# Performance work log

Hardware: AMD Instinct MI355X
Metric: run time of the kernel (lower is better)

Reference implementation:

```python
import jax, jax.numpy as jnp
import numpy as np

WINDOW_SIZE = 8
NUM_HEADS = 6
SHIFT_SIZE = 0


def rel_pos_log(ws):
    # torch.meshgrid default is 'ij' indexing
    coords = jnp.stack(jnp.meshgrid(jnp.arange(ws), jnp.arange(ws), indexing='ij'))  # [2,ws,ws]
    flat = coords.reshape(2, -1)                      # [2, N]
    rel = flat[:, :, None] - flat[:, None, :]          # [2, N, N]
    rel = rel.transpose(1, 2, 0).astype(jnp.float32)   # [N, N, 2]
    return jnp.sign(rel) * jnp.log1p(jnp.abs(rel))


def setup_inputs() -> dict:
    key = jax.random.key(0)
    k0, k1, k2, k3 = jax.random.split(key, 4)
    B_, N, dim, H = 2048, WINDOW_SIZE * WINDOW_SIZE, 192, NUM_HEADS
    qkv = jax.random.normal(k0, (B_, N, 3 * dim), dtype=jnp.float32)
    qkv_mfif = jax.random.normal(k1, (B_, N, 3 * dim), dtype=jnp.float32)
    W1 = jax.random.normal(k2, (2, 256), dtype=jnp.float32) * 0.1
    b1 = jnp.zeros((256,), dtype=jnp.float32)
    W2 = jax.random.normal(k3, (256, H), dtype=jnp.float32) * 0.1
    b2 = jnp.zeros((H,), dtype=jnp.float32)
    return {"qkv": qkv, "qkv_mfif": qkv_mfif, "W1": W1, "b1": b1,
            "W2": W2, "b2": b2, "trainingTag": 2}


def _split_heads(t, H):
    B_, N, C3 = t.shape
    dim = C3 // 3
    hd = dim // H
    t = t.reshape(B_, N, 3, H, hd).transpose(2, 0, 3, 1, 4)  # [3, B_, H, N, hd]
    return t[0], t[1], t[2]


def _forward(qkv, qkv_mfif, W1, b1, W2, b2, trainingTag):
    sg = jax.lax.stop_gradient
    H = NUM_HEADS
    B_, N, C3 = qkv.shape
    dim = C3 // 3
    hd = dim // H
    scale = hd ** (-0.5)

    q, k, v = _split_heads(qkv, H)
    qm, km, vm = _split_heads(qkv_mfif, H)

    # relative position bias from tiny MLP: [N,N,2] -> [N,N,H] -> [H,N,N]
    rp = rel_pos_log(WINDOW_SIZE)
    bias = jax.nn.relu(rp @ W1 + b1) @ W2 + b2
    bias = bias.transpose(2, 0, 1)[None]  # [1,H,N,N]

    if trainingTag == 2:
        q = sg(q * scale)
        qm = qm * scale
        if SHIFT_SIZE == 0:
            attn = sg(jnp.einsum('bhnd,bhmd->bhnm', qm, k))
        else:
            attn = sg(jnp.einsum('bhnd,bhmd->bhnm', q, k))
        attn_m = jnp.einsum('bhnd,bhmd->bhnm', qm, km)
        attn = sg(jax.nn.softmax(attn + sg(bias), axis=-1))
        attn_m = jax.nn.softmax(attn_m + bias, axis=-1)
        x_ivif = sg(jnp.einsum('bhnm,bhmd->bhnd', attn, v).transpose(0, 2, 1, 3).reshape(B_, N, dim))
        x_mfif = jnp.einsum('bhnm,bhmd->bhnd', attn_m, vm).transpose(0, 2, 1, 3).reshape(B_, N, dim)
    else:  # trainingTag == 1
        q = q * scale
        qm = sg(qm * scale)
        attn = jnp.einsum('bhnd,bhmd->bhnm', q, k)
        if SHIFT_SIZE == 0:
            attn_m = sg(jnp.einsum('bhnd,bhmd->bhnm', q, km))
        else:
            attn_m = sg(jnp.einsum('bhnd,bhmd->bhnm', qm, km))
        attn = jax.nn.softmax(attn + bias, axis=-1)
        attn_m = sg(jax.nn.softmax(attn_m + bias, axis=-1))
        x_ivif = jnp.einsum('bhnm,bhmd->bhnd', attn, v).transpose(0, 2, 1, 3).reshape(B_, N, dim)
        x_mfif = sg(jnp.einsum('bhnm,bhmd->bhnd', attn_m, vm).transpose(0, 2, 1, 3).reshape(B_, N, dim))
    return x_ivif, x_mfif


def reference(qkv, qkv_mfif, W1, b1, W2, b2, trainingTag):
    return _forward(qkv, qkv_mfif, W1, b1, W2, b2, trainingTag)
```

## Files before the change

### kernel.cpp

```cpp
#include <hip/hip_runtime.h>


typedef float  f32x4  __attribute__((ext_vector_type(4)));
typedef short  bf16x8 __attribute__((ext_vector_type(8)));
typedef unsigned short u16x8 __attribute__((ext_vector_type(8)));
typedef unsigned short u16x4 __attribute__((ext_vector_type(4)));

__device__ __forceinline__ unsigned short f2bf(float f) {
  unsigned int u = __builtin_bit_cast(unsigned int, f);
  unsigned int r = (u + 0x7FFFu + ((u >> 16) & 1u)) >> 16;
  return (unsigned short)r;
}

__global__ void bias_mlp_kernel(const float* __restrict__ W1,
                                const float* __restrict__ b1,
                                const float* __restrict__ W2,
                                const float* __restrict__ b2,
                                float* __restrict__ bias_ws) {
  int idx  = blockIdx.x * 256 + threadIdx.x;
  int reg  = idx & 3;
  int lane = (idx >> 2) & 63;
  int tile = (idx >> 8) & 15;
  int h    = idx >> 12;
  int mt = tile >> 2, nt = tile & 3;
  int n = nt * 16 + (lane & 15);
  int m = mt * 16 + (lane >> 4) * 4 + reg;
  float dr = (float)((n >> 3) - (m >> 3));
  float dc = (float)((n & 7) - (m & 7));
  float fr = copysignf(log1pf(fabsf(dr)), dr);
  float fc = copysignf(log1pf(fabsf(dc)), dc);
  float acc = b2[h];
  for (int jj = 0; jj < 256; ++jj) {
    float hid = fmaf(fr, W1[jj], fmaf(fc, W1[256 + jj], b1[jj]));
    hid = fmaxf(hid, 0.0f);
    acc = fmaf(hid, W2[jj * 6 + h], acc);
  }
  bias_ws[idx] = acc;
}

__global__ __launch_bounds__(256, 6)
void wattn_kernel(const float* __restrict__ qkv,
                  const float* __restrict__ mfif,
                  const float* __restrict__ bias_ws,
                  const int*   __restrict__ tagp,
                  float* __restrict__ out) {
  const int bid  = blockIdx.x;
  const int h    = bid % 6;
  const int b    = bid / 6;
  const int tid  = threadIdx.x;
  const int lane = tid & 63;
  const int w    = tid >> 6;
  const int j    = lane & 15;
  const int g    = lane >> 4;

  __shared__ unsigned short k_s [64][36];
  __shared__ unsigned short km_s[64][36];
  __shared__ unsigned short vT_s[2][32][66];
  __shared__ unsigned short P_s [64][66];

  const int tag = *tagp;
  const float* qsrc = (tag == 2) ? mfif : qkv;
  const size_t base = (size_t)b * 36864;
  const float scale = 0.17677669529663687f;

  bf16x8 bq;
  {
    const float* pq = qsrc + base + (size_t)(16 * w + j) * 576 + h * 32 + g * 8;
    f32x4 q0 = *(const f32x4*)pq;
    f32x4 q1 = *(const f32x4*)(pq + 4);
    u16x8 oq;
#pragma unroll
    for (int e = 0; e < 4; ++e) {
      oq[e]     = f2bf(q0[e] * scale);
      oq[e + 4] = f2bf(q1[e] * scale);
    }
    bq = __builtin_bit_cast(bf16x8, oq);
  }

  {
    const int n = tid >> 2, seg = tid & 3;
    const float* pk = qkv  + base + (size_t)n * 576 + 192 + h * 32 + seg * 8;
    const float* pm = mfif + base + (size_t)n * 576 + 192 + h * 32 + seg * 8;
    f32x4 k0 = *(const f32x4*)pk;  f32x4 k1 = *(const f32x4*)(pk + 4);
    f32x4 m0 = *(const f32x4*)pm;  f32x4 m1 = *(const f32x4*)(pm + 4);
    u16x8 ok, om;
#pragma unroll
    for (int e = 0; e < 4; ++e) {
      ok[e] = f2bf(k0[e]);  ok[e + 4] = f2bf(k1[e]);
      om[e] = f2bf(m0[e]);  om[e + 4] = f2bf(m1[e]);
    }
    *(u16x8*)&k_s [n][seg * 8] = ok;
    *(u16x8*)&km_s[n][seg * 8] = om;
  }
  {
    const int d  = tid & 31;
    const int m0 = (tid >> 5) * 8;
    const float* pv  = qkv  + base + 384 + h * 32 + d;
    const float* pvm = mfif + base + 384 + h * 32 + d;
    u16x8 ov, om;
#pragma unroll
    for (int e = 0; e < 8; ++e) {
      ov[e] = f2bf(pv [(size_t)(m0 + e) * 576]);
      om[e] = f2bf(pvm[(size_t)(m0 + e) * 576]);
    }
    *(u16x8*)&vT_s[0][d][m0] = ov;
    *(u16x8*)&vT_s[1][d][m0] = om;
  }

  f32x4 bias4[4];
#pragma unroll
  for (int mt = 0; mt < 4; ++mt)
    bias4[mt] = *(const f32x4*)&bias_ws[(((h * 16) + mt * 4 + w) * 64 + lane) * 4];

  __syncthreads();

#pragma unroll
  for (int s = 0; s < 2; ++s) {
    const unsigned short (*Ks)[36] = (s == 0) ? k_s : km_s;

    f32x4 acc[4];
#pragma unroll
    for (int mt = 0; mt < 4; ++mt) {
      bf16x8 ak = *(const bf16x8*)&Ks[mt * 16 + j][g * 8];
      acc[mt] = __builtin_amdgcn_mfma_f32_16x16x32_bf16(ak, bq, bias4[mt], 0, 0, 0);
    }

    float mx = -3.0e38f;
#pragma unroll
    for (int mt = 0; mt < 4; ++mt)
#pragma unroll
      for (int r = 0; r < 4; ++r) mx = fmaxf(mx, acc[mt][r]);
    mx = fmaxf(mx, __shfl_xor(mx, 16));
    mx = fmaxf(mx, __shfl_xor(mx, 32));
    float p[16];
    float sum = 0.0f;
#pragma unroll
    for (int mt = 0; mt < 4; ++mt)
#pragma unroll
      for (int r = 0; r < 4; ++r) {
        float e = __expf(acc[mt][r] - mx);
        p[mt * 4 + r] = e;
        sum += e;
      }
    sum += __shfl_xor(sum, 16);
    sum += __shfl_xor(sum, 32);
    const float inv = 1.0f / sum;

#pragma unroll
    for (int mt = 0; mt < 4; ++mt) {
      u16x4 pw;
#pragma unroll
      for (int r = 0; r < 4; ++r) pw[r] = f2bf(p[mt * 4 + r] * inv);
      *(u16x4*)&P_s[16 * w + j][mt * 16 + g * 4] = pw;
    }

    f32x4 xo[2] = {{0.f, 0.f, 0.f, 0.f}, {0.f, 0.f, 0.f, 0.f}};
#pragma unroll
    for (int kt = 0; kt < 2; ++kt) {
      bf16x8 ap = *(const bf16x8*)&P_s[16 * w + j][kt * 32 + g * 8];
#pragma unroll
      for (int dt = 0; dt < 2; ++dt) {
        bf16x8 bv = *(const bf16x8*)&vT_s[s][16 * dt + j][kt * 32 + g * 8];
        xo[dt] = __builtin_amdgcn_mfma_f32_16x16x32_bf16(ap, bv, xo[dt], 0, 0, 0);
      }
    }

    float* ob = out + (size_t)s * 25165824 + (size_t)b * 12288 + h * 32;
#pragma unroll
    for (int dt = 0; dt < 2; ++dt)
#pragma unroll
      for (int r = 0; r < 4; ++r)
        ob[(16 * w + g * 4 + r) * 192 + dt * 16 + j] = xo[dt][r];
  }
}

extern "C" void kernel_launch(void* const* d_in, const int* in_sizes, int n_in,
                              void* d_out, int out_size, void* d_ws, size_t ws_size,
                              hipStream_t stream) {
  const float* qkv  = (const float*)d_in[0];
  const float* mfif = (const float*)d_in[1];
  const float* W1   = (const float*)d_in[2];
  const float* b1   = (const float*)d_in[3];
  const float* W2   = (const float*)d_in[4];
  const float* b2   = (const float*)d_in[5];
  const int*   tag  = (const int*)d_in[6];
  float* out     = (float*)d_out;
  float* bias_ws = (float*)d_ws;

  hipLaunchKernelGGL(bias_mlp_kernel, dim3(96), dim3(256), 0, stream,
                     W1, b1, W2, b2, bias_ws);
  hipLaunchKernelGGL(wattn_kernel, dim3(12288), dim3(256), 0, stream,
                     qkv, mfif, bias_ws, tag, out);
}
```

Baseline: 157.4 us.

## Process all heads per block with register-prefetched next-head loads

Each block now handles one window and loops over all six heads, cutting the grid from 12288 to 2048 blocks. Global loads for the next head are issued into registers before the current head's compute, software-pipelining memory latency behind the MFMA and softmax work. Launch bounds drop to 4 blocks per SM to allow more registers for the prefetch buffers. The cost is lower occupancy, less parallelism across heads, and two extra barriers per head.

```diff
diff --git a/kernel.cpp b/kernel.cpp
--- a/kernel.cpp
+++ b/kernel.cpp
@@ -38,15 +38,12 @@
   bias_ws[idx] = acc;
 }
 
-__global__ __launch_bounds__(256, 6)
+__global__ __launch_bounds__(256, 4)
 void wattn_kernel(const float* __restrict__ qkv,
                   const float* __restrict__ mfif,
                   const float* __restrict__ bias_ws,
                   const int*   __restrict__ tagp,
                   float* __restrict__ out) {
-  const int bid  = blockIdx.x;
-  const int h    = bid % 6;
-  const int b    = bid / 6;
   const int tid  = threadIdx.x;
   const int lane = tid & 63;
   const int w    = tid >> 6;
@@ -60,117 +57,136 @@
 
   const int tag = *tagp;
   const float* qsrc = (tag == 2) ? mfif : qkv;
-  const size_t base = (size_t)b * 36864;
+  const size_t base = (size_t)blockIdx.x * 36864;
   const float scale = 0.17677669529663687f;
 
-  bf16x8 bq;
-  {
-    const float* pq = qsrc + base + (size_t)(16 * w + j) * 576 + h * 32 + g * 8;
-    f32x4 q0 = *(const f32x4*)pq;
-    f32x4 q1 = *(const f32x4*)(pq + 4);
-    u16x8 oq;
+  const int q_row = 16 * w + j;
+  const int n_k   = tid >> 2, seg = tid & 3;
+  const int d_v   = tid & 31, m0_v = (tid >> 5) * 8;
+
+  const float* qrow_p  = qsrc + base + (size_t)q_row * 576 + g * 8;
+  const float* krow_p  = qkv  + base + (size_t)n_k * 576 + 192 + seg * 8;
+  const float* mrow_p  = mfif + base + (size_t)n_k * 576 + 192 + seg * 8;
+  const float* vcol_p  = qkv  + base + 384 + d_v;
+  const float* vmcol_p = mfif + base + 384 + d_v;
+
+  f32x4 qA, qB, kA, kB, mA, mB;
+  float vv[8], vmv[8];
+
+  auto ISSUE = [&](int hh) {
+    const float* pq = qrow_p + hh * 32;
+    qA = *(const f32x4*)pq;        qB = *(const f32x4*)(pq + 4);
+    const float* pk = krow_p + hh * 32;
+    kA = *(const f32x4*)pk;        kB = *(const f32x4*)(pk + 4);
+    const float* pm = mrow_p + hh * 32;
+    mA = *(const f32x4*)pm;        mB = *(const f32x4*)(pm + 4);
+    const float* pv  = vcol_p  + hh * 32;
+    const float* pvm = vmcol_p + hh * 32;
+#pragma unroll
+    for (int e = 0; e < 8; ++e) {
+      vv[e]  = pv [(size_t)(m0_v + e) * 576];
+      vmv[e] = pvm[(size_t)(m0_v + e) * 576];
+    }
+  };
+
+  ISSUE(0);
+
+#pragma unroll 1
+  for (int hh = 0; hh < 6; ++hh) {
+    bf16x8 bq;
+    {
+      u16x8 oq;
+#pragma unroll
+      for (int e = 0; e < 4; ++e) {
+        oq[e]     = f2bf(qA[e] * scale);
+        oq[e + 4] = f2bf(qB[e] * scale);
+      }
+      bq = __builtin_bit_cast(bf16x8, oq);
+    }
+    u16x8 ok, om, ov, ovm;
 #pragma unroll
     for (int e = 0; e < 4; ++e) {
-      oq[e]     = f2bf(q0[e] * scale);
-      oq[e + 4] = f2bf(q1[e] * scale);
-    }
-    bq = __builtin_bit_cast(bf16x8, oq);
-  }
-
-  {
-    const int n = tid >> 2, seg = tid & 3;
-    const float* pk = qkv  + base + (size_t)n * 576 + 192 + h * 32 + seg * 8;
-    const float* pm = mfif + base + (size_t)n * 576 + 192 + h * 32 + seg * 8;
-    f32x4 k0 = *(const f32x4*)pk;  f32x4 k1 = *(const f32x4*)(pk + 4);
-    f32x4 m0 = *(const f32x4*)pm;  f32x4 m1 = *(const f32x4*)(pm + 4);
-    u16x8 ok, om;
-#pragma unroll
-    for (int e = 0; e < 4; ++e) {
-      ok[e] = f2bf(k0[e]);  ok[e + 4] = f2bf(k1[e]);
-      om[e] = f2bf(m0[e]);  om[e + 4] = f2bf(m1[e]);
-    }
-    *(u16x8*)&k_s [n][seg * 8] = ok;
-    *(u16x8*)&km_s[n][seg * 8] = om;
-  }
-  {
-    const int d  = tid & 31;
-    const int m0 = (tid >> 5) * 8;
-    const float* pv  = qkv  + base + 384 + h * 32 + d;
-    const float* pvm = mfif + base + 384 + h * 32 + d;
-    u16x8 ov, om;
+      ok[e] = f2bf(kA[e]);  ok[e + 4] = f2bf(kB[e]);
+      om[e] = f2bf(mA[e]);  om[e + 4] = f2bf(mB[e]);
+    }
 #pragma unroll
     for (int e = 0; e < 8; ++e) {
-      ov[e] = f2bf(pv [(size_t)(m0 + e) * 576]);
-      om[e] = f2bf(pvm[(size_t)(m0 + e) * 576]);
-    }
-    *(u16x8*)&vT_s[0][d][m0] = ov;
-    *(u16x8*)&vT_s[1][d][m0] = om;
-  }
-
-  f32x4 bias4[4];
-#pragma unroll
-  for (int mt = 0; mt < 4; ++mt)
-    bias4[mt] = *(const f32x4*)&bias_ws[(((h * 16) + mt * 4 + w) * 64 + lane) * 4];
-
-  __syncthreads();
-
-#pragma unroll
-  for (int s = 0; s < 2; ++s) {
-    const unsigned short (*Ks)[36] = (s == 0) ? k_s : km_s;
-
-    f32x4 acc[4];
-#pragma unroll
-    for (int mt = 0; mt < 4; ++mt) {
-      bf16x8 ak = *(const bf16x8*)&Ks[mt * 16 + j][g * 8];
-      acc[mt] = __builtin_amdgcn_mfma_f32_16x16x32_bf16(ak, bq, bias4[mt], 0, 0, 0);
-    }
-
-    float mx = -3.0e38f;
+      ov[e]  = f2bf(vv[e]);
+      ovm[e] = f2bf(vmv[e]);
+    }
+
+    __syncthreads();
+    *(u16x8*)&k_s [n_k][seg * 8] = ok;
+    *(u16x8*)&km_s[n_k][seg * 8] = om;
+    *(u16x8*)&vT_s[0][d_v][m0_v] = ov;
+    *(u16x8*)&vT_s[1][d_v][m0_v] = ovm;
+    __syncthreads();
+
+    if (hh < 5) ISSUE(hh + 1);
+
+    f32x4 bias4[4];
 #pragma unroll
     for (int mt = 0; mt < 4; ++mt)
-#pragma unroll
-      for (int r = 0; r < 4; ++r) mx = fmaxf(mx, acc[mt][r]);
-    mx = fmaxf(mx, __shfl_xor(mx, 16));
-    mx = fmaxf(mx, __shfl_xor(mx, 32));
-    float p[16];
-    float sum = 0.0f;
-#pragma unroll
-    for (int mt = 0; mt < 4; ++mt)
-#pragma unroll
-      for (int r = 0; r < 4; ++r) {
-        float e = __expf(acc[mt][r] - mx);
-        p[mt * 4 + r] = e;
-        sum += e;
-      }
-    sum += __shfl_xor(sum, 16);
-    sum += __shfl_xor(sum, 32);
-    const float inv = 1.0f / sum;
-
-#pragma unroll
-    for (int mt = 0; mt < 4; ++mt) {
-      u16x4 pw;
-#pragma unroll
-      for (int r = 0; r < 4; ++r) pw[r] = f2bf(p[mt * 4 + r] * inv);
-      *(u16x4*)&P_s[16 * w + j][mt * 16 + g * 4] = pw;
-    }
-
-    f32x4 xo[2] = {{0.f, 0.f, 0.f, 0.f}, {0.f, 0.f, 0.f, 0.f}};
-#pragma unroll
-    for (int kt = 0; kt < 2; ++kt) {
-      bf16x8 ap = *(const bf16x8*)&P_s[16 * w + j][kt * 32 + g * 8];
-#pragma unroll
-      for (int dt = 0; dt < 2; ++dt) {
-        bf16x8 bv = *(const bf16x8*)&vT_s[s][16 * dt + j][kt * 32 + g * 8];
-        xo[dt] = __builtin_amdgcn_mfma_f32_16x16x32_bf16(ap, bv, xo[dt], 0, 0, 0);
-      }
-    }
-
-    float* ob = out + (size_t)s * 25165824 + (size_t)b * 12288 + h * 32;
-#pragma unroll
-    for (int dt = 0; dt < 2; ++dt)
-#pragma unroll
-      for (int r = 0; r < 4; ++r)
-        ob[(16 * w + g * 4 + r) * 192 + dt * 16 + j] = xo[dt][r];
+      bias4[mt] = *(const f32x4*)&bias_ws[(((hh * 16) + mt * 4 + w) * 64 + lane) * 4];
+
+#pragma unroll
+    for (int s = 0; s < 2; ++s) {
+      const unsigned short (*Ks)[36] = (s == 0) ? k_s : km_s;
+
+      f32x4 acc[4];
+#pragma unroll
+      for (int mt = 0; mt < 4; ++mt) {
+        bf16x8 ak = *(const bf16x8*)&Ks[mt * 16 + j][g * 8];
+        acc[mt] = __builtin_amdgcn_mfma_f32_16x16x32_bf16(ak, bq, bias4[mt], 0, 0, 0);
+      }
+
+      float mx = -3.0e38f;
+#pragma unroll
+      for (int mt = 0; mt < 4; ++mt)
+#pragma unroll
+        for (int r = 0; r < 4; ++r) mx = fmaxf(mx, acc[mt][r]);
+      mx = fmaxf(mx, __shfl_xor(mx, 16));
+      mx = fmaxf(mx, __shfl_xor(mx, 32));
+      float p[16];
+      float sum = 0.0f;
+#pragma unroll
+      for (int mt = 0; mt < 4; ++mt)
+#pragma unroll
+        for (int r = 0; r < 4; ++r) {
+          float e = __expf(acc[mt][r] - mx);
+          p[mt * 4 + r] = e;
+          sum += e;
+        }
+      sum += __shfl_xor(sum, 16);
+      sum += __shfl_xor(sum, 32);
+      const float inv = 1.0f / sum;
+
+#pragma unroll
+      for (int mt = 0; mt < 4; ++mt) {
+        u16x4 pw;
+#pragma unroll
+        for (int r = 0; r < 4; ++r) pw[r] = f2bf(p[mt * 4 + r] * inv);
+        *(u16x4*)&P_s[16 * w + j][mt * 16 + g * 4] = pw;
+      }
+
+      f32x4 xo[2] = {{0.f, 0.f, 0.f, 0.f}, {0.f, 0.f, 0.f, 0.f}};
+#pragma unroll
+      for (int kt = 0; kt < 2; ++kt) {
+        bf16x8 ap = *(const bf16x8*)&P_s[16 * w + j][kt * 32 + g * 8];
+#pragma unroll
+        for (int dt = 0; dt < 2; ++dt) {
+          bf16x8 bv = *(const bf16x8*)&vT_s[s][16 * dt + j][kt * 32 + g * 8];
+          xo[dt] = __builtin_amdgcn_mfma_f32_16x16x32_bf16(ap, bv, xo[dt], 0, 0, 0);
+        }
+      }
+
+      float* ob = out + (size_t)s * 25165824 + (size_t)blockIdx.x * 12288 + hh * 32;
+#pragma unroll
+      for (int dt = 0; dt < 2; ++dt)
+#pragma unroll
+        for (int r = 0; r < 4; ++r)
+          ob[(16 * w + g * 4 + r) * 192 + dt * 16 + j] = xo[dt][r];
+    }
   }
 }
 
@@ -189,6 +205,6 @@
 
   hipLaunchKernelGGL(bias_mlp_kernel, dim3(96), dim3(256), 0, stream,
                      W1, b1, W2, b2, bias_ws);
-  hipLaunchKernelGGL(wattn_kernel, dim3(12288), dim3(256), 0, stream,
+  hipLaunchKernelGGL(wattn_kernel, dim3(2048), dim3(256), 0, stream,
                      qkv, mfif, bias_ws, tag, out);
 }
```

Result: slower. 176.9 us (+12.4%).

## Load K straight into MFMA registers and defer softmax normalization

Applied to the files above, without the earlier changes.

The K and K_mfif tiles are no longer staged through shared memory: each lane loads its own K fragment from global memory, converts it to bf16 and feeds it directly into the QK^T MFMA. V loads are issued before the softmax so their latency overlaps it. The row max is dropped, unnormalized exponentials are written to P, and the reciprocal of the row sum is applied to the output after the PV MFMA. Together with the smaller shared-memory footprint and a launch bound raised from 6 to 8 waves, this aims for more overlap and higher occupancy, at the cost of overflow risk in exp when logits are large.

```diff
diff --git a/kernel.cpp b/kernel.cpp
--- a/kernel.cpp
+++ b/kernel.cpp
@@ -38,7 +38,7 @@
   bias_ws[idx] = acc;
 }
 
-__global__ __launch_bounds__(256, 6)
+__global__ __launch_bounds__(256, 8)
 void wattn_kernel(const float* __restrict__ qkv,
                   const float* __restrict__ mfif,
                   const float* __restrict__ bias_ws,
@@ -53,124 +53,165 @@
   const int j    = lane & 15;
   const int g    = lane >> 4;
 
-  __shared__ unsigned short k_s [64][36];
-  __shared__ unsigned short km_s[64][36];
   __shared__ unsigned short vT_s[2][32][66];
   __shared__ unsigned short P_s [64][66];
+  __shared__ __align__(16) float sums_s[2][64];
 
   const int tag = *tagp;
   const float* qsrc = (tag == 2) ? mfif : qkv;
   const size_t base = (size_t)b * 36864;
   const float scale = 0.17677669529663687f;
 
-  bf16x8 bq;
+  f32x4 qA, qB;
   {
     const float* pq = qsrc + base + (size_t)(16 * w + j) * 576 + h * 32 + g * 8;
-    f32x4 q0 = *(const f32x4*)pq;
-    f32x4 q1 = *(const f32x4*)(pq + 4);
-    u16x8 oq;
-#pragma unroll
-    for (int e = 0; e < 4; ++e) {
-      oq[e]     = f2bf(q0[e] * scale);
-      oq[e + 4] = f2bf(q1[e] * scale);
-    }
-    bq = __builtin_bit_cast(bf16x8, oq);
-  }
-
-  {
-    const int n = tid >> 2, seg = tid & 3;
-    const float* pk = qkv  + base + (size_t)n * 576 + 192 + h * 32 + seg * 8;
-    const float* pm = mfif + base + (size_t)n * 576 + 192 + h * 32 + seg * 8;
-    f32x4 k0 = *(const f32x4*)pk;  f32x4 k1 = *(const f32x4*)(pk + 4);
-    f32x4 m0 = *(const f32x4*)pm;  f32x4 m1 = *(const f32x4*)(pm + 4);
-    u16x8 ok, om;
-#pragma unroll
-    for (int e = 0; e < 4; ++e) {
-      ok[e] = f2bf(k0[e]);  ok[e + 4] = f2bf(k1[e]);
-      om[e] = f2bf(m0[e]);  om[e + 4] = f2bf(m1[e]);
-    }
-    *(u16x8*)&k_s [n][seg * 8] = ok;
-    *(u16x8*)&km_s[n][seg * 8] = om;
-  }
-  {
-    const int d  = tid & 31;
-    const int m0 = (tid >> 5) * 8;
-    const float* pv  = qkv  + base + 384 + h * 32 + d;
-    const float* pvm = mfif + base + 384 + h * 32 + d;
-    u16x8 ov, om;
-#pragma unroll
-    for (int e = 0; e < 8; ++e) {
-      ov[e] = f2bf(pv [(size_t)(m0 + e) * 576]);
-      om[e] = f2bf(pvm[(size_t)(m0 + e) * 576]);
-    }
-    *(u16x8*)&vT_s[0][d][m0] = ov;
-    *(u16x8*)&vT_s[1][d][m0] = om;
-  }
-
+    qA = *(const f32x4*)pq;
+    qB = *(const f32x4*)(pq + 4);
+  }
   f32x4 bias4[4];
 #pragma unroll
   for (int mt = 0; mt < 4; ++mt)
     bias4[mt] = *(const f32x4*)&bias_ws[(((h * 16) + mt * 4 + w) * 64 + lane) * 4];
 
-  __syncthreads();
-
-#pragma unroll
-  for (int s = 0; s < 2; ++s) {
-    const unsigned short (*Ks)[36] = (s == 0) ? k_s : km_s;
-
-    f32x4 acc[4];
+  const float* kb0 = qkv + base + 192 + h * 32 + (size_t)j * 576 + g * 8;
+
+  bf16x8 bq;
+  {
+    u16x8 oq;
+#pragma unroll
+    for (int e = 0; e < 4; ++e) {
+      oq[e]     = f2bf(qA[e] * scale);
+      oq[e + 4] = f2bf(qB[e] * scale);
+    }
+    bq = __builtin_bit_cast(bf16x8, oq);
+  }
+
+  f32x4 acc[4];
+#pragma unroll
+  for (int mt = 0; mt < 4; ++mt) {
+    f32x4 a0 = *(const f32x4*)(kb0 + (size_t)mt * 9216);
+    f32x4 a1 = *(const f32x4*)(kb0 + (size_t)mt * 9216 + 4);
+    u16x8 ok;
+#pragma unroll
+    for (int e = 0; e < 4; ++e) { ok[e] = f2bf(a0[e]); ok[e + 4] = f2bf(a1[e]); }
+    acc[mt] = __builtin_amdgcn_mfma_f32_16x16x32_bf16(
+        __builtin_bit_cast(bf16x8, ok), bq, bias4[mt], 0, 0, 0);
+  }
+
+  const int d_v = tid & 31, m0_v = (tid >> 5) * 8;
+  const float* pv  = qkv  + base + 384 + h * 32 + d_v;
+  const float* pvm = mfif + base + 384 + h * 32 + d_v;
+  float vv[8], vmv[8];
+#pragma unroll
+  for (int e = 0; e < 8; ++e) vv[e]  = pv [(size_t)(m0_v + e) * 576];
+#pragma unroll
+  for (int e = 0; e < 8; ++e) vmv[e] = pvm[(size_t)(m0_v + e) * 576];
+
+  {
+    float t0 = 0.f, t1 = 0.f, t2 = 0.f, t3 = 0.f;
 #pragma unroll
     for (int mt = 0; mt < 4; ++mt) {
-      bf16x8 ak = *(const bf16x8*)&Ks[mt * 16 + j][g * 8];
-      acc[mt] = __builtin_amdgcn_mfma_f32_16x16x32_bf16(ak, bq, bias4[mt], 0, 0, 0);
-    }
-
-    float mx = -3.0e38f;
-#pragma unroll
-    for (int mt = 0; mt < 4; ++mt)
-#pragma unroll
-      for (int r = 0; r < 4; ++r) mx = fmaxf(mx, acc[mt][r]);
-    mx = fmaxf(mx, __shfl_xor(mx, 16));
-    mx = fmaxf(mx, __shfl_xor(mx, 32));
-    float p[16];
-    float sum = 0.0f;
-#pragma unroll
-    for (int mt = 0; mt < 4; ++mt)
-#pragma unroll
-      for (int r = 0; r < 4; ++r) {
-        float e = __expf(acc[mt][r] - mx);
-        p[mt * 4 + r] = e;
-        sum += e;
-      }
+      float e0 = __expf(acc[mt][0]);
+      float e1 = __expf(acc[mt][1]);
+      float e2 = __expf(acc[mt][2]);
+      float e3 = __expf(acc[mt][3]);
+      u16x4 pw;
+      pw[0] = f2bf(e0); pw[1] = f2bf(e1); pw[2] = f2bf(e2); pw[3] = f2bf(e3);
+      *(u16x4*)&P_s[16 * w + j][mt * 16 + g * 4] = pw;
+      t0 += e0; t1 += e1; t2 += e2; t3 += e3;
+    }
+    float sum = (t0 + t1) + (t2 + t3);
     sum += __shfl_xor(sum, 16);
     sum += __shfl_xor(sum, 32);
-    const float inv = 1.0f / sum;
-
-#pragma unroll
-    for (int mt = 0; mt < 4; ++mt) {
-      u16x4 pw;
-#pragma unroll
-      for (int r = 0; r < 4; ++r) pw[r] = f2bf(p[mt * 4 + r] * inv);
-      *(u16x4*)&P_s[16 * w + j][mt * 16 + g * 4] = pw;
-    }
-
+    if (g == 0) sums_s[0][16 * w + j] = sum;
+  }
+
+  {
+    u16x8 ov, om;
+#pragma unroll
+    for (int e = 0; e < 8; ++e) { ov[e] = f2bf(vv[e]); om[e] = f2bf(vmv[e]); }
+    *(u16x8*)&vT_s[0][d_v][m0_v] = ov;
+    *(u16x8*)&vT_s[1][d_v][m0_v] = om;
+  }
+  __syncthreads();
+
+  {
     f32x4 xo[2] = {{0.f, 0.f, 0.f, 0.f}, {0.f, 0.f, 0.f, 0.f}};
 #pragma unroll
     for (int kt = 0; kt < 2; ++kt) {
       bf16x8 ap = *(const bf16x8*)&P_s[16 * w + j][kt * 32 + g * 8];
 #pragma unroll
       for (int dt = 0; dt < 2; ++dt) {
-        bf16x8 bv = *(const bf16x8*)&vT_s[s][16 * dt + j][kt * 32 + g * 8];
+        bf16x8 bv = *(const bf16x8*)&vT_s[0][16 * dt + j][kt * 32 + g * 8];
         xo[dt] = __builtin_amdgcn_mfma_f32_16x16x32_bf16(ap, bv, xo[dt], 0, 0, 0);
       }
     }
-
-    float* ob = out + (size_t)s * 25165824 + (size_t)b * 12288 + h * 32;
+    f32x4 sm = *(const f32x4*)&sums_s[0][16 * w + 4 * g];
+    float inv[4];
+#pragma unroll
+    for (int r = 0; r < 4; ++r) inv[r] = __builtin_amdgcn_rcpf(sm[r]);
+    float* ob = out + (size_t)b * 12288 + h * 32;
 #pragma unroll
     for (int dt = 0; dt < 2; ++dt)
 #pragma unroll
       for (int r = 0; r < 4; ++r)
-        ob[(16 * w + g * 4 + r) * 192 + dt * 16 + j] = xo[dt][r];
+        ob[(16 * w + g * 4 + r) * 192 + dt * 16 + j] = xo[dt][r] * inv[r];
+  }
+
+  {
+    const float* kb1 = mfif + base + 192 + h * 32 + (size_t)j * 576 + g * 8;
+    f32x4 acm[4];
+#pragma unroll
+    for (int mt = 0; mt < 4; ++mt) {
+      f32x4 a0 = *(const f32x4*)(kb1 + (size_t)mt * 9216);
+      f32x4 a1 = *(const f32x4*)(kb1 + (size_t)mt * 9216 + 4);
+      u16x8 ok;
+#pragma unroll
+      for (int e = 0; e < 4; ++e) { ok[e] = f2bf(a0[e]); ok[e + 4] = f2bf(a1[e]); }
+      acm[mt] = __builtin_amdgcn_mfma_f32_16x16x32_bf16(
+          __builtin_bit_cast(bf16x8, ok), bq, bias4[mt], 0, 0, 0);
+    }
+    float t0 = 0.f, t1 = 0.f, t2 = 0.f, t3 = 0.f;
+    u16x4 pw1[4];
+#pragma unroll
+    for (int mt = 0; mt < 4; ++mt) {
+      float e0 = __expf(acm[mt][0]);
+      float e1 = __expf(acm[mt][1]);
+      float e2 = __expf(acm[mt][2]);
+      float e3 = __expf(acm[mt][3]);
+      pw1[mt][0] = f2bf(e0); pw1[mt][1] = f2bf(e1);
+      pw1[mt][2] = f2bf(e2); pw1[mt][3] = f2bf(e3);
+      t0 += e0; t1 += e1; t2 += e2; t3 += e3;
+    }
+    float sum = (t0 + t1) + (t2 + t3);
+    sum += __shfl_xor(sum, 16);
+    sum += __shfl_xor(sum, 32);
+    if (g == 0) sums_s[1][16 * w + j] = sum;
+
+#pragma unroll
+    for (int mt = 0; mt < 4; ++mt)
+      *(u16x4*)&P_s[16 * w + j][mt * 16 + g * 4] = pw1[mt];
+
+    f32x4 xo[2] = {{0.f, 0.f, 0.f, 0.f}, {0.f, 0.f, 0.f, 0.f}};
+#pragma unroll
+    for (int kt = 0; kt < 2; ++kt) {
+      bf16x8 ap = *(const bf16x8*)&P_s[16 * w + j][kt * 32 + g * 8];
+#pragma unroll
+      for (int dt = 0; dt < 2; ++dt) {
+        bf16x8 bv = *(const bf16x8*)&vT_s[1][16 * dt + j][kt * 32 + g * 8];
+        xo[dt] = __builtin_amdgcn_mfma_f32_16x16x32_bf16(ap, bv, xo[dt], 0, 0, 0);
+      }
+    }
+    f32x4 sm = *(const f32x4*)&sums_s[1][16 * w + 4 * g];
+    float inv[4];
+#pragma unroll
+    for (int r = 0; r < 4; ++r) inv[r] = __builtin_amdgcn_rcpf(sm[r]);
+    float* ob = out + 25165824 + (size_t)b * 12288 + h * 32;
+#pragma unroll
+    for (int dt = 0; dt < 2; ++dt)
+#pragma unroll
+      for (int r = 0; r < 4; ++r)
+        ob[(16 * w + g * 4 + r) * 192 + dt * 16 + j] = xo[dt][r] * inv[r];
   }
 }
 
```

Measured after the change: 266.7 us. +69.5%, slower.

## Process two heads per block with wider loads and deferred softmax normalization

Applied to the files above, without the earlier changes.

Each block now handles a pair of heads. This halves the grid and lets K and V rows be loaded as contiguous 64-float spans with float4 loads. The block index is remapped so neighbouring work lands on the same XCD. Softmax no longer subtracts the row max; normalization by the reciprocal of the row sum is moved to the output store, with row sums passed through shared memory. The aim is to cut memory-transaction and ALU overhead in a bandwidth-bound kernel, at the cost of lower occupancy and a risk of exp overflow for large scores.

```diff
diff --git a/kernel.cpp b/kernel.cpp
--- a/kernel.cpp
+++ b/kernel.cpp
@@ -38,139 +38,163 @@
   bias_ws[idx] = acc;
 }
 
-__global__ __launch_bounds__(256, 6)
+__global__ __launch_bounds__(256, 3)
 void wattn_kernel(const float* __restrict__ qkv,
                   const float* __restrict__ mfif,
                   const float* __restrict__ bias_ws,
                   const int*   __restrict__ tagp,
                   float* __restrict__ out) {
-  const int bid  = blockIdx.x;
-  const int h    = bid % 6;
-  const int b    = bid / 6;
+  const int nb   = blockIdx.x;
+  const int orig = (nb & 7) * 768 + (nb >> 3);
+  const int b    = orig / 3;
+  const int hp   = orig - 3 * b;
   const int tid  = threadIdx.x;
   const int lane = tid & 63;
   const int w    = tid >> 6;
   const int j    = lane & 15;
   const int g    = lane >> 4;
 
-  __shared__ unsigned short k_s [64][36];
-  __shared__ unsigned short km_s[64][36];
-  __shared__ unsigned short vT_s[2][32][66];
+  __shared__ unsigned short k_s [2][64][36];
+  __shared__ unsigned short km_s[2][64][36];
+  __shared__ unsigned short vT_s[2][2][32][72];
   __shared__ unsigned short P_s [64][66];
+  __shared__ __align__(16) float sums_s[2][64];
 
   const int tag = *tagp;
   const float* qsrc = (tag == 2) ? mfif : qkv;
   const size_t base = (size_t)b * 36864;
   const float scale = 0.17677669529663687f;
 
-  bf16x8 bq;
+  const int rl  = lane >> 4;
+  const int c16 = lane & 15;
+  const float* kbp = qkv  + base + (size_t)(16 * w + rl) * 576 + 192 + 64 * hp + c16 * 4;
+  const float* mbp = mfif + base + (size_t)(16 * w + rl) * 576 + 192 + 64 * hp + c16 * 4;
+  f32x4 kf0 = *(const f32x4*)(kbp);
+  f32x4 kf1 = *(const f32x4*)(kbp + 4 * 576);
+  f32x4 kf2 = *(const f32x4*)(kbp + 8 * 576);
+  f32x4 kf3 = *(const f32x4*)(kbp + 12 * 576);
+  f32x4 mf0 = *(const f32x4*)(mbp);
+  f32x4 mf1 = *(const f32x4*)(mbp + 4 * 576);
+  f32x4 mf2 = *(const f32x4*)(mbp + 8 * 576);
+  f32x4 mf3 = *(const f32x4*)(mbp + 12 * 576);
+
+  const float* vbp  = qkv  + base + (size_t)(16 * w) * 576 + 384 + 64 * hp + lane;
+  const float* vmbp = mfif + base + (size_t)(16 * w) * 576 + 384 + 64 * hp + lane;
+  float vv[16], vmv[16];
+#pragma unroll
+  for (int e = 0; e < 16; ++e) {
+    vv[e]  = vbp [(size_t)e * 576];
+    vmv[e] = vmbp[(size_t)e * 576];
+  }
+
+  const int hl = c16 >> 3;
+  const int cc = (c16 & 7) * 4;
   {
-    const float* pq = qsrc + base + (size_t)(16 * w + j) * 576 + h * 32 + g * 8;
-    f32x4 q0 = *(const f32x4*)pq;
-    f32x4 q1 = *(const f32x4*)(pq + 4);
-    u16x8 oq;
-#pragma unroll
-    for (int e = 0; e < 4; ++e) {
-      oq[e]     = f2bf(q0[e] * scale);
-      oq[e + 4] = f2bf(q1[e] * scale);
+    u16x4 t0, t1;
+#pragma unroll
+    for (int e = 0; e < 4; ++e) { t0[e] = f2bf(kf0[e]); t1[e] = f2bf(mf0[e]); }
+    *(u16x4*)&k_s [hl][16 * w + 0 + rl][cc] = t0;
+    *(u16x4*)&km_s[hl][16 * w + 0 + rl][cc] = t1;
+#pragma unroll
+    for (int e = 0; e < 4; ++e) { t0[e] = f2bf(kf1[e]); t1[e] = f2bf(mf1[e]); }
+    *(u16x4*)&k_s [hl][16 * w + 4 + rl][cc] = t0;
+    *(u16x4*)&km_s[hl][16 * w + 4 + rl][cc] = t1;
+#pragma unroll
+    for (int e = 0; e < 4; ++e) { t0[e] = f2bf(kf2[e]); t1[e] = f2bf(mf2[e]); }
+    *(u16x4*)&k_s [hl][16 * w + 8 + rl][cc] = t0;
+    *(u16x4*)&km_s[hl][16 * w + 8 + rl][cc] = t1;
+#pragma unroll
+    for (int e = 0; e < 4; ++e) { t0[e] = f2bf(kf3[e]); t1[e] = f2bf(mf3[e]); }
+    *(u16x4*)&k_s [hl][16 * w + 12 + rl][cc] = t0;
+    *(u16x4*)&km_s[hl][16 * w + 12 + rl][cc] = t1;
+  }
+  {
+    const int hv = lane >> 5, dd = lane & 31;
+    u16x8 a0, a1, b0, b1;
+#pragma unroll
+    for (int e = 0; e < 8; ++e) {
+      a0[e] = f2bf(vv[e]);      a1[e] = f2bf(vv[8 + e]);
+      b0[e] = f2bf(vmv[e]);     b1[e] = f2bf(vmv[8 + e]);
     }
-    bq = __builtin_bit_cast(bf16x8, oq);
-  }
-
-  {
-    const int n = tid >> 2, seg = tid & 3;
-    const float* pk = qkv  + base + (size_t)n * 576 + 192 + h * 32 + seg * 8;
-    const float* pm = mfif + base + (size_t)n * 576 + 192 + h * 32 + seg * 8;
-    f32x4 k0 = *(const f32x4*)pk;  f32x4 k1 = *(const f32x4*)(pk + 4);
-    f32x4 m0 = *(const f32x4*)pm;  f32x4 m1 = *(const f32x4*)(pm + 4);
-    u16x8 ok, om;
-#pragma unroll
-    for (int e = 0; e < 4; ++e) {
-      ok[e] = f2bf(k0[e]);  ok[e + 4] = f2bf(k1[e]);
-      om[e] = f2bf(m0[e]);  om[e + 4] = f2bf(m1[e]);
+    *(u16x8*)&vT_s[hv][0][dd][16 * w]     = a0;
+    *(u16x8*)&vT_s[hv][0][dd][16 * w + 8] = a1;
+    *(u16x8*)&vT_s[hv][1][dd][16 * w]     = b0;
+    *(u16x8*)&vT_s[hv][1][dd][16 * w + 8] = b1;
+  }
+  __syncthreads();
+
+#pragma unroll
+  for (int h2 = 0; h2 < 2; ++h2) {
+    const int h = 2 * hp + h2;
+
+    bf16x8 bq;
+    {
+      const float* pq = qsrc + base + (size_t)(16 * w + j) * 576 + h * 32 + g * 8;
+      f32x4 qA = *(const f32x4*)pq;
+      f32x4 qB = *(const f32x4*)(pq + 4);
+      u16x8 oq;
+#pragma unroll
+      for (int e = 0; e < 4; ++e) {
+        oq[e]     = f2bf(qA[e] * scale);
+        oq[e + 4] = f2bf(qB[e] * scale);
+      }
+      bq = __builtin_bit_cast(bf16x8, oq);
     }
-    *(u16x8*)&k_s [n][seg * 8] = ok;
-    *(u16x8*)&km_s[n][seg * 8] = om;
-  }
-  {
-    const int d  = tid & 31;
-    const int m0 = (tid >> 5) * 8;
-    const float* pv  = qkv  + base + 384 + h * 32 + d;
-    const float* pvm = mfif + base + 384 + h * 32 + d;
-    u16x8 ov, om;
-#pragma unroll
-    for (int e = 0; e < 8; ++e) {
-      ov[e] = f2bf(pv [(size_t)(m0 + e) * 576]);
-      om[e] = f2bf(pvm[(size_t)(m0 + e) * 576]);
+    f32x4 bias4[4];
+#pragma unroll
+    for (int mt = 0; mt < 4; ++mt)
+      bias4[mt] = *(const f32x4*)&bias_ws[(((h * 16) + mt * 4 + w) * 64 + lane) * 4];
+
+#pragma unroll
+    for (int s = 0; s < 2; ++s) {
+      const unsigned short (*Ks)[36] = (s == 0) ? k_s[h2] : km_s[h2];
+
+      f32x4 acc[4];
+#pragma unroll
+      for (int mt = 0; mt < 4; ++mt) {
+        bf16x8 ak = *(const bf16x8*)&Ks[mt * 16 + j][g * 8];
+        acc[mt] = __builtin_amdgcn_mfma_f32_16x16x32_bf16(ak, bq, bias4[mt], 0, 0, 0);
+      }
+
+      float t0 = 0.f, t1 = 0.f, t2 = 0.f, t3 = 0.f;
+#pragma unroll
+      for (int mt = 0; mt < 4; ++mt) {
+        float e0 = __expf(acc[mt][0]);
+        float e1 = __expf(acc[mt][1]);
+        float e2 = __expf(acc[mt][2]);
+        float e3 = __expf(acc[mt][3]);
+        u16x4 pw;
+        pw[0] = f2bf(e0); pw[1] = f2bf(e1); pw[2] = f2bf(e2); pw[3] = f2bf(e3);
+        *(u16x4*)&P_s[16 * w + j][mt * 16 + g * 4] = pw;
+        t0 += e0; t1 += e1; t2 += e2; t3 += e3;
+      }
+      float sum = (t0 + t1) + (t2 + t3);
+      sum += __shfl_xor(sum, 16);
+      sum += __shfl_xor(sum, 32);
+      if (g == 0) sums_s[s][16 * w + j] = sum;
+
+      f32x4 xo[2] = {{0.f, 0.f, 0.f, 0.f}, {0.f, 0.f, 0.f, 0.f}};
+#pragma unroll
+      for (int kt = 0; kt < 2; ++kt) {
+        bf16x8 ap = *(const bf16x8*)&P_s[16 * w + j][kt * 32 + g * 8];
+#pragma unroll
+        for (int dt = 0; dt < 2; ++dt) {
+          bf16x8 bv = *(const bf16x8*)&vT_s[h2][s][16 * dt + j][kt * 32 + g * 8];
+          xo[dt] = __builtin_amdgcn_mfma_f32_16x16x32_bf16(ap, bv, xo[dt], 0, 0, 0);
+        }
+      }
+
+      f32x4 sm = *(const f32x4*)&sums_s[s][16 * w + 4 * g];
+      float inv[4];
+#pragma unroll
+      for (int r = 0; r < 4; ++r) inv[r] = __builtin_amdgcn_rcpf(sm[r]);
+      float* ob = out + (size_t)s * 25165824 + (size_t)b * 12288 + h * 32;
+#pragma unroll
+      for (int dt = 0; dt < 2; ++dt)
+#pragma unroll
+        for (int r = 0; r < 4; ++r)
+          ob[(16 * w + g * 4 + r) * 192 + dt * 16 + j] = xo[dt][r] * inv[r];
     }
-    *(u16x8*)&vT_s[0][d][m0] = ov;
-    *(u16x8*)&vT_s[1][d][m0] = om;
-  }
-
-  f32x4 bias4[4];
-#pragma unroll
-  for (int mt = 0; mt < 4; ++mt)
-    bias4[mt] = *(const f32x4*)&bias_ws[(((h * 16) + mt * 4 + w) * 64 + lane) * 4];
-
-  __syncthreads();
-
-#pragma unroll
-  for (int s = 0; s < 2; ++s) {
-    const unsigned short (*Ks)[36] = (s == 0) ? k_s : km_s;
-
-    f32x4 acc[4];
-#pragma unroll
-    for (int mt = 0; mt < 4; ++mt) {
-      bf16x8 ak = *(const bf16x8*)&Ks[mt * 16 + j][g * 8];
-      acc[mt] = __builtin_amdgcn_mfma_f32_16x16x32_bf16(ak, bq, bias4[mt], 0, 0, 0);
-    }
-
-    float mx = -3.0e38f;
-#pragma unroll
-    for (int mt = 0; mt < 4; ++mt)
-#pragma unroll
-      for (int r = 0; r < 4; ++r) mx = fmaxf(mx, acc[mt][r]);
-    mx = fmaxf(mx, __shfl_xor(mx, 16));
-    mx = fmaxf(mx, __shfl_xor(mx, 32));
-    float p[16];
-    float sum = 0.0f;
-#pragma unroll
-    for (int mt = 0; mt < 4; ++mt)
-#pragma unroll
-      for (int r = 0; r < 4; ++r) {
-        float e = __expf(acc[mt][r] - mx);
-        p[mt * 4 + r] = e;
-        sum += e;
-      }
-    sum += __shfl_xor(sum, 16);
-    sum += __shfl_xor(sum, 32);
-    const float inv = 1.0f / sum;
-
-#pragma unroll
-    for (int mt = 0; mt < 4; ++mt) {
-      u16x4 pw;
-#pragma unroll
-      for (int r = 0; r < 4; ++r) pw[r] = f2bf(p[mt * 4 + r] * inv);
-      *(u16x4*)&P_s[16 * w + j][mt * 16 + g * 4] = pw;
-    }
-
-    f32x4 xo[2] = {{0.f, 0.f, 0.f, 0.f}, {0.f, 0.f, 0.f, 0.f}};
-#pragma unroll
-    for (int kt = 0; kt < 2; ++kt) {
-      bf16x8 ap = *(const bf16x8*)&P_s[16 * w + j][kt * 32 + g * 8];
-#pragma unroll
-      for (int dt = 0; dt < 2; ++dt) {
-        bf16x8 bv = *(const bf16x8*)&vT_s[s][16 * dt + j][kt * 32 + g * 8];
-        xo[dt] = __builtin_amdgcn_mfma_f32_16x16x32_bf16(ap, bv, xo[dt], 0, 0, 0);
-      }
-    }
-
-    float* ob = out + (size_t)s * 25165824 + (size_t)b * 12288 + h * 32;
-#pragma unroll
-    for (int dt = 0; dt < 2; ++dt)
-#pragma unroll
-      for (int r = 0; r < 4; ++r)
-        ob[(16 * w + g * 4 + r) * 192 + dt * 16 + j] = xo[dt][r];
   }
 }
 
@@ -189,6 +213,6 @@
 
   hipLaunchKernelGGL(bias_mlp_kernel, dim3(96), dim3(256), 0, stream,
                      W1, b1, W2, b2, bias_ws);
-  hipLaunchKernelGGL(wattn_kernel, dim3(12288), dim3(256), 0, stream,
+  hipLaunchKernelGGL(wattn_kernel, dim3(6144), dim3(256), 0, stream,
                      qkv, mfif, bias_ws, tag, out);
 }
```

Result: no change. 159.4 us (+1.3%).
